# Performance work log

Hardware: AMD Instinct MI355X
Metric: run time of the kernel (lower is better)

Reference implementation:

```python
import jax, jax.numpy as jnp
import numpy as np

B, S, E, D, H = 4, 1024, 1024, 1024, 16   # batch, dec_seq, enc_seq, d_model, n_heads
DH = D // H
DFF = 4096
EPS = 1e-5


def setup_inputs() -> dict:
    key = jax.random.key(0)
    ks = jax.random.split(key, 16)
    w = lambda k, shp: (jax.random.normal(k, shp, dtype=jnp.float32) * 0.02)
    return {
        "x": jax.random.normal(ks[0], (B, S, D), dtype=jnp.float32),
        "enc_x": jax.random.normal(ks[1], (B, E, D), dtype=jnp.float32),
        # masked self-attn (fused qkv)
        "w_qkv": w(ks[2], (D, 3 * D)), "b_qkv": jnp.zeros((3 * D,), jnp.float32),
        "w_sa_o": w(ks[3], (D, D)), "b_sa_o": jnp.zeros((D,), jnp.float32),
        # cross-attn
        "w_q": w(ks[4], (D, D)), "b_q": jnp.zeros((D,), jnp.float32),
        "w_k": w(ks[5], (D, D)), "b_k": jnp.zeros((D,), jnp.float32),
        "w_v": w(ks[6], (D, D)), "b_v": jnp.zeros((D,), jnp.float32),
        "w_ca_o": w(ks[7], (D, D)), "b_ca_o": jnp.zeros((D,), jnp.float32),
        # ffn
        "w1": w(ks[8], (D, DFF)), "b1": jnp.zeros((DFF,), jnp.float32),
        "w2": w(ks[9], (DFF, D)), "b2": jnp.zeros((D,), jnp.float32),
        # layernorms
        "g1": jnp.ones((D,), jnp.float32), "be1": jnp.zeros((D,), jnp.float32),
        "g2": jnp.ones((D,), jnp.float32), "be2": jnp.zeros((D,), jnp.float32),
        "g3": jnp.ones((D,), jnp.float32), "be3": jnp.zeros((D,), jnp.float32),
    }


def _layernorm(x, g, b):
    mean = jnp.mean(x, axis=-1, keepdims=True)
    var = jnp.mean(jnp.square(x - mean), axis=-1, keepdims=True)  # unbiased=False
    return g * (x - mean) / jnp.sqrt(var + EPS) + b


def _masked_self_attn(x, w_qkv, b_qkv, w_o, b_o):
    b, s, d = x.shape
    qkv = x @ w_qkv + b_qkv                            # [b,s,3D]
    # Faithful to torch: view as [b,s,H,3*DH] then chunk last dim (interleaved per-head).
    qkv = qkv.reshape(b, s, H, 3 * DH).transpose(0, 2, 1, 3)   # [b,H,s,3DH]
    q, k, v = jnp.split(qkv, 3, axis=-1)               # each [b,H,s,DH]
    scores = jnp.einsum('bhqd,bhkd->bhqk', q, k) / jnp.sqrt(jnp.float32(DH))
    mask = jnp.triu(jnp.ones((s, s), dtype=bool), k=1)
    scores = jnp.where(mask, -jnp.inf, scores)
    attn = jax.nn.softmax(scores, axis=-1)
    out = jnp.einsum('bhqk,bhkd->bhqd', attn, v)       # [b,H,s,DH]
    out = out.transpose(0, 2, 1, 3).reshape(b, s, d)
    return out @ w_o + b_o


def _cross_attn(dec_x, enc_x, w_q, b_q, w_k, b_k, w_v, b_v, w_o, b_o):
    b, sq, d = dec_x.shape
    sk = enc_x.shape[1]
    q = (dec_x @ w_q + b_q).reshape(b, sq, H, DH).transpose(0, 2, 1, 3)
    k = (enc_x @ w_k + b_k).reshape(b, sk, H, DH).transpose(0, 2, 1, 3)
    v = (enc_x @ w_v + b_v).reshape(b, sk, H, DH).transpose(0, 2, 1, 3)
    scores = jnp.einsum('bhqd,bhkd->bhqk', q, k) / jnp.sqrt(jnp.float32(DH))
    attn = jax.nn.softmax(scores, axis=-1)
    out = jnp.einsum('bhqk,bhkd->bhqd', attn, v).transpose(0, 2, 1, 3).reshape(b, sq, d)
    return out @ w_o + b_o


def reference(x, enc_x, w_qkv, b_qkv, w_sa_o, b_sa_o,
              w_q, b_q, w_k, b_k, w_v, b_v, w_ca_o, b_ca_o,
              w1, b1, w2, b2, g1, be1, g2, be2, g3, be3):
    h = _layernorm(x + _masked_self_attn(x, w_qkv, b_qkv, w_sa_o, b_sa_o), g1, be1)
    h = _layernorm(h + _cross_attn(h, enc_x, w_q, b_q, w_k, b_k, w_v, b_v, w_ca_o, b_ca_o), g2, be2)
    ffn = jax.nn.gelu(h @ w1 + b1, approximate=False) @ w2 + b2  # torch F.gelu default = exact
    return _layernorm(h + ffn, g3, be3)
```

## Files before the change

kernel.cpp:

```cpp
#include <hip/hip_runtime.h>

#define BB 4
#define SS 1024
#define DD 1024
#define HH 16
#define DHH 64
#define DFF 4096
#define MROWS 4096
#define NEG_BIG (-1e30f)
#define LOG2E 1.4426950408889634f
#define SCL_L2E 0.1803368801111244f

typedef float  f32x4  __attribute__((ext_vector_type(4)));
typedef __bf16 bf16x8 __attribute__((ext_vector_type(8)));
typedef __bf16 bf16x4 __attribute__((ext_vector_type(4)));

#define DEV __device__ __forceinline__

DEV void glds16(const __bf16* g, __bf16* l) {
  __builtin_amdgcn_global_load_lds((__attribute__((address_space(1))) void*)(g),
                                   (__attribute__((address_space(3))) void*)(l),
                                   16, 0, 0);
}

DEV float sanit(float v) {
  return fminf(fmaxf(v, -1e30f), 1e30f);
}

DEV float gelu_f(float v) {
  const float z  = fabsf(v) * 0.70710678118654752f;
  const float t  = __builtin_amdgcn_rcpf(1.f + 0.3275911f * z);
  float poly = ((((1.061405429f * t - 1.453152027f) * t + 1.421413741f) * t
                 - 0.284496736f) * t + 0.254829592f) * t;
  float er = 1.f - poly * __expf(-z * z);
  er = copysignf(er, v);
  return 0.5f * v * (1.f + er);
}

__global__ __launch_bounds__(256) void cvt_bf16(const float* __restrict__ src,
                                                __bf16* __restrict__ dst)
{
  const int idx = blockIdx.x * 256 + threadIdx.x;
  const f32x4 v = ((const f32x4*)src)[idx];
  bf16x4 o;
#pragma unroll
  for (int i = 0; i < 4; i++) o[i] = (__bf16)v[i];
  ((bf16x4*)dst)[idx] = o;
}

__global__ __launch_bounds__(256) void wtrans(const float* __restrict__ src,
                                              __bf16* __restrict__ dst,
                                              int K, int N)
{
  __shared__ float t[64][65];
  const int k0 = blockIdx.y * 64, n0 = blockIdx.x * 64;
  const int c = threadIdx.x & 63, r0 = threadIdx.x >> 6;
#pragma unroll
  for (int i = 0; i < 16; i++) {
    const int r = r0 * 16 + i;
    t[r][c] = src[(size_t)(k0 + r) * N + n0 + c];
  }
  __syncthreads();
#pragma unroll
  for (int i = 0; i < 16; i++) {
    const int r = r0 * 16 + i;
    dst[(size_t)(n0 + r) * K + k0 + c] = (__bf16)t[c][r];
  }
}

__global__ __launch_bounds__(256) void vtrans(const __bf16* __restrict__ src,
                                              int stride, int colMul, int colAdd,
                                              __bf16* __restrict__ dst)
{
  __shared__ __bf16 t[64][66];
  const int bh = blockIdx.y, b = bh >> 4, h = bh & 15;
  const int s0 = blockIdx.x * 64;
  const int c = threadIdx.x & 63, r0 = threadIdx.x >> 6;
  const __bf16* sp = src + (size_t)(b * SS) * stride + h * colMul + colAdd;
#pragma unroll
  for (int i = 0; i < 16; i++) {
    const int s = r0 * 16 + i;
    t[s][c] = sp[(size_t)(s0 + s) * stride + c];
  }
  __syncthreads();
  __bf16* dp = dst + (size_t)bh * 64 * 1024;
#pragma unroll
  for (int i = 0; i < 16; i++) {
    const int d = r0 * 16 + i;
    dp[(size_t)d * 1024 + s0 + c] = t[c][d];
  }
}

template<int MODE>
__global__ __launch_bounds__(256) void gemm_bt(
    const __bf16* __restrict__ A, const __bf16* __restrict__ Bt,
    const float* __restrict__ bias, const float* __restrict__ bias2,
    void* __restrict__ Cout, int N, int K)
{
  __shared__ __align__(16) __bf16 As[2][128 * 32];
  __shared__ __align__(16) __bf16 Bs[2][128 * 32];

  const int bm = blockIdx.y * 128, bn = blockIdx.x * 128;
  const int tid = threadIdx.x, wid = tid >> 6, lane = tid & 63;
  const int quad = lane >> 4, ln = lane & 15;

  const __bf16* gA = A  + (size_t)(bm + wid * 32 + (lane >> 2)) * K + (lane & 3) * 8;
  const __bf16* gB = Bt + (size_t)(bn + wid * 32 + (lane >> 2)) * K + (lane & 3) * 8;
  const int soff = (wid * 32) * 32;

  f32x4 acc[4][4];
#pragma unroll
  for (int i = 0; i < 4; i++)
#pragma unroll
    for (int j = 0; j < 4; j++) acc[i][j] = (f32x4){0.f, 0.f, 0.f, 0.f};

  const int wr = (wid >> 1) * 64, wc = (wid & 1) * 64;

#define G_STAGE(buf, kt) do {                                     \
    const int k0_ = (kt) * 32;                                    \
    glds16(gA + k0_,          &As[buf][soff]);                    \
    glds16(gA + 16 * K + k0_, &As[buf][soff + 16 * 32]);          \
    glds16(gB + k0_,          &Bs[buf][soff]);                    \
    glds16(gB + 16 * K + k0_, &Bs[buf][soff + 16 * 32]);          \
  } while (0)

#define G_COMP(buf) do {                                                    \
    bf16x8 af[4], bfr[4];                                                   \
    _Pragma("unroll")                                                       \
    for (int i = 0; i < 4; i++)                                             \
      af[i] = *(const bf16x8*)(&As[buf][(wr + i * 16 + ln) * 32 + quad * 8]); \
    _Pragma("unroll")                                                       \
    for (int j = 0; j < 4; j++)                                             \
      bfr[j] = *(const bf16x8*)(&Bs[buf][(wc + j * 16 + ln) * 32 + quad * 8]); \
    _Pragma("unroll")                                                       \
    for (int i = 0; i < 4; i++)                                             \
      _Pragma("unroll")                                                     \
      for (int j = 0; j < 4; j++)                                           \
        acc[i][j] = __builtin_amdgcn_mfma_f32_16x16x32_bf16(af[i], bfr[j], acc[i][j], 0, 0, 0); \
  } while (0)

  const int nk = K >> 5;
  G_STAGE(0, 0);
  __syncthreads();
  for (int kt = 0; kt < nk; kt += 2) {
    G_STAGE(1, kt + 1);
    G_COMP(0);
    __syncthreads();
    if (kt + 2 < nk) G_STAGE(0, kt + 2);
    G_COMP(1);
    __syncthreads();
  }
#undef G_STAGE
#undef G_COMP

#pragma unroll
  for (int j = 0; j < 4; j++) {
    const int col = bn + wc + j * 16 + ln;
    float bv;
    if (MODE == 4) bv = (col < 1024) ? bias[col] : bias2[col - 1024];
    else           bv = bias[col];
#pragma unroll
    for (int i = 0; i < 4; i++) {
#pragma unroll
      for (int r = 0; r < 4; r++) {
        const int row = bm + wr + i * 16 + quad * 4 + r;
        float v = sanit(acc[i][j][r] + bv);
        if (MODE == 1) v = gelu_f(v);
        if (MODE == 3 && (col % 192) < 64) v *= SCL_L2E;
        if (MODE == 2) ((float*)Cout)[(size_t)row * N + col] = v;
        else           ((__bf16*)Cout)[(size_t)row * N + col] = (__bf16)v;
      }
    }
  }
}

template<int MODE, int SPLIT>
__global__ __launch_bounds__(256) void gemm_bt64(
    const __bf16* __restrict__ A, const __bf16* __restrict__ Bt,
    const float* __restrict__ bias, void* __restrict__ Cout,
    int N, int K)
{
  __shared__ __align__(16) __bf16 As[2][128 * 32];
  __shared__ __align__(16) __bf16 Bs[2][64 * 32];

  const int bm = blockIdx.y * 128, bn = blockIdx.x * 64;
  const int kz = SPLIT ? blockIdx.z : 0;
  const int kOff = SPLIT ? kz * (K >> 1) : 0;
  const int tid = threadIdx.x, wid = tid >> 6, lane = tid & 63;
  const int quad = lane >> 4, ln = lane & 15;

  const __bf16* gA = A  + (size_t)(bm + wid * 32 + (lane >> 2)) * K + (lane & 3) * 8 + kOff;
  const __bf16* gB = Bt + (size_t)(bn + wid * 16 + (lane >> 2)) * K + (lane & 3) * 8 + kOff;
  const int aoff = (wid * 32) * 32;
  const int boff = (wid * 16) * 32;

  f32x4 acc[4][2];
#pragma unroll
  for (int i = 0; i < 4; i++)
#pragma unroll
    for (int j = 0; j < 2; j++) acc[i][j] = (f32x4){0.f, 0.f, 0.f, 0.f};

  const int wr = (wid >> 1) * 64, wc = (wid & 1) * 32;

#define G_STAGE(buf, kt) do {                                     \
    const int k0_ = (kt) * 32;                                    \
    glds16(gA + k0_,          &As[buf][aoff]);                    \
    glds16(gA + 16 * K + k0_, &As[buf][aoff + 16 * 32]);          \
    glds16(gB + k0_,          &Bs[buf][boff]);                    \
  } while (0)

#define G_COMP(buf) do {                                                    \
    bf16x8 af[4], bfr[2];                                                   \
    _Pragma("unroll")                                                       \
    for (int i = 0; i < 4; i++)                                             \
      af[i] = *(const bf16x8*)(&As[buf][(wr + i * 16 + ln) * 32 + quad * 8]); \
    _Pragma("unroll")                                                       \
    for (int j = 0; j < 2; j++)                                             \
      bfr[j] = *(const bf16x8*)(&Bs[buf][(wc + j * 16 + ln) * 32 + quad * 8]); \
    _Pragma("unroll")                                                       \
    for (int i = 0; i < 4; i++)                                             \
      _Pragma("unroll")                                                     \
      for (int j = 0; j < 2; j++)                                           \
        acc[i][j] = __builtin_amdgcn_mfma_f32_16x16x32_bf16(af[i], bfr[j], acc[i][j], 0, 0, 0); \
  } while (0)

  const int nk = (K >> SPLIT) >> 5;
  G_STAGE(0, 0);
  __syncthreads();
  for (int kt = 0; kt < nk; kt += 2) {
    G_STAGE(1, kt + 1);
    G_COMP(0);
    __syncthreads();
    if (kt + 2 < nk) G_STAGE(0, kt + 2);
    G_COMP(1);
    __syncthreads();
  }
#undef G_STAGE
#undef G_COMP

  float* outF = (float*)Cout + (SPLIT ? (size_t)kz * MROWS * N : 0);
#pragma unroll
  for (int j = 0; j < 2; j++) {
    const int col = bn + wc + j * 16 + ln;
    const float bv = (SPLIT && kz) ? 0.f : bias[col];
#pragma unroll
    for (int i = 0; i < 4; i++) {
#pragma unroll
      for (int r = 0; r < 4; r++) {
        const int row = bm + wr + i * 16 + quad * 4 + r;
        float v = sanit(acc[i][j][r] + bv);
        if (MODE == 3) v *= SCL_L2E;
        if (MODE == 2) outF[(size_t)row * N + col] = v;
        else           ((__bf16*)Cout)[(size_t)row * N + col] = (__bf16)v;
      }
    }
  }
}

__global__ __launch_bounds__(256) void attn(
    const __bf16* __restrict__ qp, int qStride, int qMul, int qAdd,
    const __bf16* __restrict__ kp, int kStride, int kMul, int kAdd,
    const __bf16* __restrict__ vt, __bf16* __restrict__ outp, int causal)
{
  __shared__ __align__(16) __bf16 Kt[2][64 * 64];
  __shared__ __align__(16) __bf16 Vt[2][64 * 64];
  __shared__ __align__(16) __bf16 ptl[4][32 * 64];

  const int id = blockIdx.x;
  const int bh = ((id >> 6) << 3) | (id & 7);
  const int qblk = (id >> 3) & 7;
  const int b = bh >> 4, h = bh & 15;
  const int tid = threadIdx.x, wid = tid >> 6, lane = tid & 63;
  const int quad = lane >> 4, ln = lane & 15;
  const int qbase = qblk * 128;
  const int rowb0 = qbase + wid * 32;
  const int rowTop = rowb0 + 31;

  bf16x8 aq[2][2];
#pragma unroll
  for (int rf = 0; rf < 2; ++rf) {
    const __bf16* qr = qp + (size_t)(b * SS + rowb0 + rf * 16 + ln) * qStride
                          + h * qMul + qAdd;
#pragma unroll
    for (int ks = 0; ks < 2; ++ks)
      aq[rf][ks] = *(const bf16x8*)(qr + ks * 32 + quad * 8);
  }

  f32x4 acc[2][4];
#pragma unroll
  for (int rf = 0; rf < 2; ++rf)
#pragma unroll
    for (int nb = 0; nb < 4; ++nb) acc[rf][nb] = (f32x4){0.f, 0.f, 0.f, 0.f};
  float l_r[2][4] = {{0.f,0.f,0.f,0.f},{0.f,0.f,0.f,0.f}};

  const __bf16* kbase = kp + (size_t)(b * SS) * kStride + h * kMul + kAdd;
  const __bf16* vtb = vt + (size_t)bh * 64 * 1024;
  __bf16* ptw = ptl[wid];

  const int kvEnd = causal ? (qbase + 128) : SS;
  const int nT = kvEnd >> 6;

  const int sr = wid * 16 + (lane >> 3);
  const int sq = lane & 7;

#pragma unroll
  for (int p = 0; p < 2; ++p) {
    const int r = sr + p * 8;
    const int qs = (sq ^ (r & 7)) * 8;
    glds16(kbase + (size_t)r * kStride + qs, Kt[0] + (wid * 2 + p) * 512);
    glds16(vtb + (size_t)r * 1024 + qs,      Vt[0] + (wid * 2 + p) * 512);
  }

  for (int t = 0; t < nT; ++t) {
    const int cur = t & 1;
    const int kv0 = t * 64;

    if (t + 1 < nT) {
      const int kn = kv0 + 64;
#pragma unroll
      for (int p = 0; p < 2; ++p) {
        const int r = sr + p * 8;
        const int qs = (sq ^ (r & 7)) * 8;
        glds16(kbase + (size_t)(kn + r) * kStride + qs, Kt[cur ^ 1] + (wid * 2 + p) * 512);
        glds16(vtb + (size_t)r * 1024 + kn + qs,        Vt[cur ^ 1] + (wid * 2 + p) * 512);
      }
      __asm__ volatile("s_waitcnt vmcnt(4)" ::: "memory");
    } else {
      __asm__ volatile("s_waitcnt vmcnt(0)" ::: "memory");
    }
    __builtin_amdgcn_sched_barrier(0);
    __builtin_amdgcn_s_barrier();
    __asm__ volatile("" ::: "memory");
    __builtin_amdgcn_sched_barrier(0);

    if (!causal || kv0 <= rowTop) {
      const __bf16* kt = Kt[cur];
      const __bf16* vv = Vt[cur];

      f32x4 sc[2][4];
      {
        bf16x8 kf[4][2];
#pragma unroll
        for (int c = 0; c < 4; ++c) {
          const int row = c * 16 + ln;
#pragma unroll
          for (int ks = 0; ks < 2; ++ks)
            kf[c][ks] = *(const bf16x8*)(kt + row * 64 + (((ks * 4 + quad) ^ (ln & 7)) * 8));
        }
#pragma unroll
        for (int rf = 0; rf < 2; ++rf)
#pragma unroll
          for (int c = 0; c < 4; ++c) {
            f32x4 s_ = (f32x4){0.f, 0.f, 0.f, 0.f};
            s_ = __builtin_amdgcn_mfma_f32_16x16x32_bf16(aq[rf][0], kf[c][0], s_, 0, 0, 0);
            s_ = __builtin_amdgcn_mfma_f32_16x16x32_bf16(aq[rf][1], kf[c][1], s_, 0, 0, 0);
            sc[rf][c] = s_;
          }
      }

#pragma unroll
      for (int rf = 0; rf < 2; ++rf) {
        const bool doMask = causal && (kv0 + 63 > rowb0 + rf * 16);
#pragma unroll
        for (int r = 0; r < 4; ++r) {
          const int rowg = rowb0 + rf * 16 + quad * 4 + r;
          float p[4];
#pragma unroll
          for (int c = 0; c < 4; ++c) {
            float e = sc[rf][c][r];
            if (doMask && (kv0 + c * 16 + ln > rowg)) e = NEG_BIG;
            p[c] = exp2f(e);
          }
          l_r[rf][r] += (p[0] + p[1]) + (p[2] + p[3]);
          const int m = rf * 16 + quad * 4 + r;
          __bf16* pr = ptw + m * 64;
#pragma unroll
          for (int c = 0; c < 4; ++c) {
            const int col = c * 16 + ln;
            pr[(((col >> 3) ^ (m & 7)) << 3) + (col & 7)] = (__bf16)p[c];
          }
        }
      }
      __asm__ volatile("s_waitcnt lgkmcnt(0)" ::: "memory");
      __builtin_amdgcn_sched_barrier(0);

      {
        bf16x8 pa[2][2];
#pragma unroll
        for (int rf = 0; rf < 2; ++rf) {
          const int m = rf * 16 + ln;
#pragma unroll
          for (int ks = 0; ks < 2; ++ks)
            pa[rf][ks] = *(const bf16x8*)(ptw + m * 64 + (((ks * 4 + quad) ^ (m & 7)) * 8));
        }
#pragma unroll
        for (int nb = 0; nb < 4; ++nb) {
          const int vrow = nb * 16 + ln;
          const bf16x8 vf0 = *(const bf16x8*)(vv + vrow * 64 + (((quad)     ^ (ln & 7)) * 8));
          const bf16x8 vf1 = *(const bf16x8*)(vv + vrow * 64 + (((4 + quad) ^ (ln & 7)) * 8));
#pragma unroll
          for (int rf = 0; rf < 2; ++rf) {
            acc[rf][nb] = __builtin_amdgcn_mfma_f32_16x16x32_bf16(pa[rf][0], vf0, acc[rf][nb], 0, 0, 0);
            acc[rf][nb] = __builtin_amdgcn_mfma_f32_16x16x32_bf16(pa[rf][1], vf1, acc[rf][nb], 0, 0, 0);
          }
        }
      }
    }

    __asm__ volatile("" ::: "memory");
    __builtin_amdgcn_sched_barrier(0);
    __builtin_amdgcn_s_barrier();
  }

#pragma unroll
  for (int rf = 0; rf < 2; ++rf) {
#pragma unroll
    for (int r = 0; r < 4; ++r) {
      float l = l_r[rf][r];
#pragma unroll
      for (int off = 1; off < 16; off <<= 1) l += __shfl_xor(l, off, 64);
      const float inv = 1.f / fmaxf(l, 1e-30f);
      const int rowg = rowb0 + rf * 16 + quad * 4 + r;
      __bf16* op = outp + (size_t)(b * SS + rowg) * DD + h * 64;
#pragma unroll
      for (int nb = 0; nb < 4; ++nb)
        op[nb * 16 + ln] = (__bf16)sanit(acc[rf][nb][r] * inv);
    }
  }
}

__global__ __launch_bounds__(256) void ln_k(
    const float* __restrict__ residf, const float* __restrict__ proj,
    const float* __restrict__ proj2,
    const float* __restrict__ g, const float* __restrict__ be,
    float* __restrict__ outf, __bf16* __restrict__ outb)
{
  const int row = blockIdx.x, tid = threadIdx.x;
  const f32x4 pb = ((const f32x4*)(proj   + (size_t)row * 1024))[tid];
  const f32x4 rb = ((const f32x4*)(residf + (size_t)row * 1024))[tid];
  f32x4 x;
#pragma unroll
  for (int i = 0; i < 4; i++) x[i] = pb[i] + rb[i];
  if (proj2) {
    const f32x4 qb_ = ((const f32x4*)(proj2 + (size_t)row * 1024))[tid];
#pragma unroll
    for (int i = 0; i < 4; i++) x[i] += qb_[i];
  }
#pragma unroll
  for (int i = 0; i < 4; i++)
    x[i] = fminf(fmaxf(x[i], -1e15f), 1e15f);
  float s  = x[0] + x[1] + x[2] + x[3];
  float ss = x[0]*x[0] + x[1]*x[1] + x[2]*x[2] + x[3]*x[3];
#pragma unroll
  for (int off = 1; off < 64; off <<= 1) {
    s  += __shfl_xor(s,  off, 64);
    ss += __shfl_xor(ss, off, 64);
  }
  __shared__ float sm[8];
  if ((tid & 63) == 0) { sm[tid >> 6] = s; sm[4 + (tid >> 6)] = ss; }
  __syncthreads();
  s  = sm[0] + sm[1] + sm[2] + sm[3];
  ss = sm[4] + sm[5] + sm[6] + sm[7];
  const float mean = s * (1.f / 1024.f);
  const float var  = fmaxf(ss * (1.f / 1024.f) - mean * mean, 0.f);
  const float rstd = rsqrtf(var + 1e-5f);
  const int c = tid * 4;
  f32x4 o;
#pragma unroll
  for (int i = 0; i < 4; i++)
    o[i] = g[c + i] * ((x[i] - mean) * rstd) + be[c + i];
  if (outf) ((f32x4*)(outf + (size_t)row * 1024))[tid] = o;
  if (outb) {
    bf16x4 ob;
#pragma unroll
    for (int i = 0; i < 4; i++) ob[i] = (__bf16)o[i];
    ((bf16x4*)(outb + (size_t)row * 1024))[tid] = ob;
  }
}

extern "C" void kernel_launch(void* const* d_in, const int* in_sizes, int n_in,
                              void* d_out, int out_size, void* d_ws, size_t ws_size,
                              hipStream_t stream)
{
  const float* x      = (const float*)d_in[0];
  const float* enc    = (const float*)d_in[1];
  const float* w_qkv  = (const float*)d_in[2];
  const float* b_qkv  = (const float*)d_in[3];
  const float* w_sa_o = (const float*)d_in[4];
  const float* b_sa_o = (const float*)d_in[5];
  const float* w_q    = (const float*)d_in[6];
  const float* b_q    = (const float*)d_in[7];
  const float* w_k    = (const float*)d_in[8];
  const float* b_k    = (const float*)d_in[9];
  const float* w_v    = (const float*)d_in[10];
  const float* b_v    = (const float*)d_in[11];
  const float* w_ca_o = (const float*)d_in[12];
  const float* b_ca_o = (const float*)d_in[13];
  const float* w1     = (const float*)d_in[14];
  const float* b1     = (const float*)d_in[15];
  const float* w2     = (const float*)d_in[16];
  const float* b2     = (const float*)d_in[17];
  const float* g1     = (const float*)d_in[18];
  const float* be1    = (const float*)d_in[19];
  const float* g2     = (const float*)d_in[20];
  const float* be2    = (const float*)d_in[21];
  const float* g3     = (const float*)d_in[22];
  const float* be3    = (const float*)d_in[23];

  const size_t MB = 1024 * 1024;
  char* base = (char*)d_ws;
  __bf16* wqkvT = (__bf16*)(base + 0 * MB);
  __bf16* wsaoT = (__bf16*)(base + 6 * MB);
  __bf16* wqT   = (__bf16*)(base + 8 * MB);
  __bf16* wkvT  = (__bf16*)(base + 10 * MB);
  __bf16* wkT   = (__bf16*)(base + 10 * MB);
  __bf16* wvT   = (__bf16*)(base + 12 * MB);
  __bf16* wcaoT = (__bf16*)(base + 14 * MB);
  __bf16* w1T   = (__bf16*)(base + 0 * MB);
  __bf16* w2T   = (__bf16*)(base + 8 * MB);
  __bf16* xb    = (__bf16*)(base + 16 * MB);
  __bf16* encb  = (__bf16*)(base + 24 * MB);
  __bf16* qkv   = (__bf16*)(base + 32 * MB);
  __bf16* kvb   = (__bf16*)(base + 32 * MB);
  __bf16* qcab  = (__bf16*)(base + 48 * MB);
  __bf16* vt    = (__bf16*)(base + 56 * MB);
  __bf16* mid   = (__bf16*)(base + 32 * MB);
  __bf16* attnb = (__bf16*)(base + 64 * MB);
  float*  proj  = (float*) (base + 72 * MB);
  float*  h1f   = (float*) (base + 88 * MB);
  __bf16* h1b   = (__bf16*)(base + 104 * MB);
  float*  h2f   = (float*) (base + 112 * MB);
  __bf16* h2b   = (__bf16*)(base + 128 * MB);
  __bf16* qb = qkv;
  __bf16* kb = qkv + (size_t)MROWS * 1024;
  __bf16* vb = qkv + (size_t)MROWS * 2048;
  (void)kb; (void)vb; (void)wkT; (void)wvT;

  cvt_bf16<<<4096, 256, 0, stream>>>(x,   xb);
  cvt_bf16<<<4096, 256, 0, stream>>>(enc, encb);
  wtrans<<<dim3(48, 16), 256, 0, stream>>>(w_qkv,  wqkvT, 1024, 3072);
  wtrans<<<dim3(16, 16), 256, 0, stream>>>(w_sa_o, wsaoT, 1024, 1024);
  wtrans<<<dim3(16, 16), 256, 0, stream>>>(w_q,    wqT,   1024, 1024);
  wtrans<<<dim3(16, 16), 256, 0, stream>>>(w_k,    wkT,   1024, 1024);
  wtrans<<<dim3(16, 16), 256, 0, stream>>>(w_v,    wvT,   1024, 1024);
  wtrans<<<dim3(16, 16), 256, 0, stream>>>(w_ca_o, wcaoT, 1024, 1024);

  gemm_bt<3><<<dim3(24, 32), 256, 0, stream>>>(xb, wqkvT, b_qkv, nullptr, qkv, 3072, 1024);
  vtrans<<<dim3(16, 64), 256, 0, stream>>>(qkv, 3072, 192, 128, vt);
  attn<<<512, 256, 0, stream>>>(qkv, 3072, 192, 0,
                                qkv, 3072, 192, 64, vt, attnb, 1);
  gemm_bt64<2,0><<<dim3(16, 32), 256, 0, stream>>>(attnb, wsaoT, b_sa_o, proj, 1024, 1024);
  ln_k<<<4096, 256, 0, stream>>>(x, proj, nullptr, g1, be1, h1f, h1b);

  gemm_bt64<3,0><<<dim3(16, 32), 256, 0, stream>>>(h1b, wqT, b_q, qcab, 1024, 1024);
  gemm_bt<4><<<dim3(16, 32), 256, 0, stream>>>(encb, wkvT, b_k, b_v, kvb, 2048, 1024);
  vtrans<<<dim3(16, 64), 256, 0, stream>>>(kvb, 2048, 64, 1024, vt);
  attn<<<512, 256, 0, stream>>>(qcab, 1024, 64, 0,
                                kvb, 2048, 64, 0, vt, attnb, 0);
  gemm_bt64<2,0><<<dim3(16, 32), 256, 0, stream>>>(attnb, wcaoT, b_ca_o, proj, 1024, 1024);
  ln_k<<<4096, 256, 0, stream>>>(h1f, proj, nullptr, g2, be2, h2f, h2b);

  wtrans<<<dim3(64, 16), 256, 0, stream>>>(w1, w1T, 1024, 4096);
  wtrans<<<dim3(16, 64), 256, 0, stream>>>(w2, w2T, 4096, 1024);
  gemm_bt<1><<<dim3(32, 32), 256, 0, stream>>>(h2b, w1T, b1, nullptr, mid, 4096, 1024);
  gemm_bt64<2,1><<<dim3(16, 32, 2), 256, 0, stream>>>(mid, w2T, b2, proj, 1024, 4096);
  ln_k<<<4096, 256, 0, stream>>>(h2f, proj, proj + (size_t)MROWS * 1024,
                                 g3, be3, (float*)d_out, nullptr);

  (void)in_sizes; (void)n_in; (void)out_size; (void)ws_size;
}
```

Measured before the change: 572.0 us.

## Add 256x256 tiled GEMM with 8 waves for QKV and FFN projections

Adds a 512-thread GEMM kernel that computes 256x256 output tiles with a 64-deep K step. It double-buffers LDS filled by direct global-to-LDS loads, uses an XOR-swizzled LDS layout, interleaves loads with MFMA via explicit waitcnt and barriers, raises wave priority during MFMA, and remaps workgroup IDs across the grid. The kernel replaces the 128-tile GEMMs for the fused QKV projection, FFN up-projection with GELU, and the split-K FFN down-projection, aiming for more data reuse per tile and better latency hiding. In exchange it uses larger LDS and register footprints and launches fewer workgroups: 192 for QKV, 256 for FFN1 and 128 for FFN2. That may leave compute units idle or cause a wave-quantization tail.

```diff
diff --git a/kernel.cpp b/kernel.cpp
--- a/kernel.cpp
+++ b/kernel.cpp
@@ -88,6 +88,150 @@
   for (int i = 0; i < 16; i++) {
     const int d = r0 * 16 + i;
     dp[(size_t)d * 1024 + s0 + c] = t[c][d];
+  }
+}
+
+template<int MODE, int SPLIT>
+__global__ __launch_bounds__(512) void gemm256(
+    const __bf16* __restrict__ A, const __bf16* __restrict__ Bt,
+    const float* __restrict__ bias, void* __restrict__ Cout,
+    int N, int K)
+{
+  __shared__ __align__(16) __bf16 As[2][2][2][128 * 32];
+  __shared__ __align__(16) __bf16 Bs[2][2][2][128 * 32];
+
+  const int gx = gridDim.x;
+  const int nwg = gx * gridDim.y;
+  int idl = blockIdx.x + gx * blockIdx.y;
+  idl = (idl & 7) * (nwg >> 3) + (idl >> 3);
+  const int bn = (idl % gx) * 256, bm = (idl / gx) * 256;
+  const int kz = SPLIT ? blockIdx.z : 0;
+  const int Keff = SPLIT ? (K >> 1) : K;
+  const int kOff = SPLIT ? kz * Keff : 0;
+
+  const int tid = threadIdx.x, wid = tid >> 6, lane = tid & 63;
+  const int quad = lane >> 4, ln = lane & 15;
+  const int wr = (wid >> 2) * 128, wc = (wid & 3) * 64;
+  const int mh = wid >> 2;
+  const int nh = (wid & 3) >> 1;
+  const int rbB = wc & 64;
+  const int sw = ln >> 2;
+
+  const int srow = tid >> 2;
+  const int scol = ((tid & 3) ^ ((tid >> 4) & 3)) * 8;
+  const __bf16* gA = A  + (size_t)(bm + srow) * K + kOff + scol;
+  const __bf16* gB = Bt + (size_t)(bn + srow) * K + kOff + scol;
+  const int dOff = tid * 8;
+
+#define STG(bf_, MATG, MATS, kh_, kt_) do {                                         \
+    glds16(MATG + (size_t)(kt_) * 64 + (kh_) * 32,                 &MATS[bf_][0][kh_][0] + dOff); \
+    glds16(MATG + (size_t)128 * K + (size_t)(kt_) * 64 + (kh_) * 32, &MATS[bf_][1][kh_][0] + dOff); \
+  } while (0)
+
+#define LD_A(dst, p_, i_, ks_) \
+  dst = *(const bf16x8*)(&As[p_][mh][ks_][0] + ((i_) * 16 + ln) * 32 + ((quad ^ sw) * 8))
+#define LD_B(dst, p_, j_, ks_) \
+  dst = *(const bf16x8*)(&Bs[p_][nh][ks_][0] + (rbB + (j_) * 16 + ln) * 32 + ((quad ^ sw) * 8))
+
+  f32x4 acc[8][4];
+#pragma unroll
+  for (int i = 0; i < 8; i++)
+#pragma unroll
+    for (int j = 0; j < 4; j++) acc[i][j] = (f32x4){0.f, 0.f, 0.f, 0.f};
+
+  const int nkt = Keff >> 6;
+  STG(0, gA, As, 0, 0); STG(0, gB, Bs, 0, 0);
+  STG(0, gA, As, 1, 0); STG(0, gB, Bs, 1, 0);
+
+  for (int tt = 0; tt < nkt; ++tt) {
+    const int p = tt & 1, pn = p ^ 1;
+    const int ktn = (tt + 1 < nkt) ? (tt + 1) : tt;
+    bf16x8 af[4], bfr[4];
+
+    STG(pn, gA, As, 0, ktn);
+    asm volatile("s_waitcnt vmcnt(6)" ::: "memory");
+    __builtin_amdgcn_sched_barrier(0);
+    __builtin_amdgcn_s_barrier();
+#pragma unroll
+    for (int j = 0; j < 4; j++) LD_B(bfr[j], p, j, 0);
+#pragma unroll
+    for (int i = 0; i < 4; i++) LD_A(af[i], p, i, 0);
+    asm volatile("s_waitcnt lgkmcnt(0)" ::: "memory");
+    __builtin_amdgcn_sched_barrier(0);
+    __builtin_amdgcn_s_setprio(1);
+#pragma unroll
+    for (int i = 0; i < 4; i++)
+#pragma unroll
+      for (int j = 0; j < 4; j++)
+        acc[i][j] = __builtin_amdgcn_mfma_f32_16x16x32_bf16(af[i], bfr[j], acc[i][j], 0, 0, 0);
+    __builtin_amdgcn_s_setprio(0);
+
+    STG(pn, gB, Bs, 0, ktn);
+#pragma unroll
+    for (int i = 0; i < 4; i++) LD_A(af[i], p, i + 4, 0);
+    asm volatile("s_waitcnt lgkmcnt(0)" ::: "memory");
+    __builtin_amdgcn_sched_barrier(0);
+    __builtin_amdgcn_s_setprio(1);
+#pragma unroll
+    for (int i = 0; i < 4; i++)
+#pragma unroll
+      for (int j = 0; j < 4; j++)
+        acc[i + 4][j] = __builtin_amdgcn_mfma_f32_16x16x32_bf16(af[i], bfr[j], acc[i + 4][j], 0, 0, 0);
+    __builtin_amdgcn_s_setprio(0);
+
+    STG(pn, gA, As, 1, ktn);
+    asm volatile("s_waitcnt vmcnt(6)" ::: "memory");
+    __builtin_amdgcn_sched_barrier(0);
+    __builtin_amdgcn_s_barrier();
+#pragma unroll
+    for (int j = 0; j < 4; j++) LD_B(bfr[j], p, j, 1);
+#pragma unroll
+    for (int i = 0; i < 4; i++) LD_A(af[i], p, i, 1);
+    asm volatile("s_waitcnt lgkmcnt(0)" ::: "memory");
+    __builtin_amdgcn_sched_barrier(0);
+    __builtin_amdgcn_s_setprio(1);
+#pragma unroll
+    for (int i = 0; i < 4; i++)
+#pragma unroll
+      for (int j = 0; j < 4; j++)
+        acc[i][j] = __builtin_amdgcn_mfma_f32_16x16x32_bf16(af[i], bfr[j], acc[i][j], 0, 0, 0);
+    __builtin_amdgcn_s_setprio(0);
+
+    STG(pn, gB, Bs, 1, ktn);
+#pragma unroll
+    for (int i = 0; i < 4; i++) LD_A(af[i], p, i + 4, 1);
+    asm volatile("s_waitcnt lgkmcnt(0)" ::: "memory");
+    __builtin_amdgcn_sched_barrier(0);
+    __builtin_amdgcn_s_setprio(1);
+#pragma unroll
+    for (int i = 0; i < 4; i++)
+#pragma unroll
+      for (int j = 0; j < 4; j++)
+        acc[i + 4][j] = __builtin_amdgcn_mfma_f32_16x16x32_bf16(af[i], bfr[j], acc[i + 4][j], 0, 0, 0);
+    __builtin_amdgcn_s_setprio(0);
+    __builtin_amdgcn_s_barrier();
+  }
+#undef STG
+#undef LD_A
+#undef LD_B
+
+  float* outF = (float*)Cout + (SPLIT ? (size_t)kz * MROWS * N : 0);
+#pragma unroll
+  for (int j = 0; j < 4; j++) {
+    const int col = bn + wc + j * 16 + ln;
+    const float bv = (SPLIT && kz) ? 0.f : bias[col];
+#pragma unroll
+    for (int i = 0; i < 8; i++) {
+#pragma unroll
+      for (int r = 0; r < 4; r++) {
+        const int row = bm + wr + i * 16 + quad * 4 + r;
+        float v = sanit(acc[i][j][r] + bv);
+        if (MODE == 1) v = gelu_f(v);
+        if (MODE == 3 && (col % 192) < 64) v *= SCL_L2E;
+        if (MODE == 2) outF[(size_t)row * N + col] = v;
+        else           ((__bf16*)Cout)[(size_t)row * N + col] = (__bf16)v;
+      }
+    }
   }
 }
 
@@ -174,7 +318,7 @@
   }
 }
 
-template<int MODE, int SPLIT>
+template<int MODE>
 __global__ __launch_bounds__(256) void gemm_bt64(
     const __bf16* __restrict__ A, const __bf16* __restrict__ Bt,
     const float* __restrict__ bias, void* __restrict__ Cout,
@@ -184,13 +328,11 @@
   __shared__ __align__(16) __bf16 Bs[2][64 * 32];
 
   const int bm = blockIdx.y * 128, bn = blockIdx.x * 64;
-  const int kz = SPLIT ? blockIdx.z : 0;
-  const int kOff = SPLIT ? kz * (K >> 1) : 0;
   const int tid = threadIdx.x, wid = tid >> 6, lane = tid & 63;
   const int quad = lane >> 4, ln = lane & 15;
 
-  const __bf16* gA = A  + (size_t)(bm + wid * 32 + (lane >> 2)) * K + (lane & 3) * 8 + kOff;
-  const __bf16* gB = Bt + (size_t)(bn + wid * 16 + (lane >> 2)) * K + (lane & 3) * 8 + kOff;
+  const __bf16* gA = A  + (size_t)(bm + wid * 32 + (lane >> 2)) * K + (lane & 3) * 8;
+  const __bf16* gB = Bt + (size_t)(bn + wid * 16 + (lane >> 2)) * K + (lane & 3) * 8;
   const int aoff = (wid * 32) * 32;
   const int boff = (wid * 16) * 32;
 
@@ -224,7 +366,7 @@
         acc[i][j] = __builtin_amdgcn_mfma_f32_16x16x32_bf16(af[i], bfr[j], acc[i][j], 0, 0, 0); \
   } while (0)
 
-  const int nk = (K >> SPLIT) >> 5;
+  const int nk = K >> 5;
   G_STAGE(0, 0);
   __syncthreads();
   for (int kt = 0; kt < nk; kt += 2) {
@@ -238,11 +380,10 @@
 #undef G_STAGE
 #undef G_COMP
 
-  float* outF = (float*)Cout + (SPLIT ? (size_t)kz * MROWS * N : 0);
 #pragma unroll
   for (int j = 0; j < 2; j++) {
     const int col = bn + wc + j * 16 + ln;
-    const float bv = (SPLIT && kz) ? 0.f : bias[col];
+    const float bv = bias[col];
 #pragma unroll
     for (int i = 0; i < 4; i++) {
 #pragma unroll
@@ -250,7 +391,7 @@
         const int row = bm + wr + i * 16 + quad * 4 + r;
         float v = sanit(acc[i][j][r] + bv);
         if (MODE == 3) v *= SCL_L2E;
-        if (MODE == 2) outF[(size_t)row * N + col] = v;
+        if (MODE == 2) ((float*)Cout)[(size_t)row * N + col] = v;
         else           ((__bf16*)Cout)[(size_t)row * N + col] = (__bf16)v;
       }
     }
@@ -531,10 +672,7 @@
   __bf16* h1b   = (__bf16*)(base + 104 * MB);
   float*  h2f   = (float*) (base + 112 * MB);
   __bf16* h2b   = (__bf16*)(base + 128 * MB);
-  __bf16* qb = qkv;
-  __bf16* kb = qkv + (size_t)MROWS * 1024;
-  __bf16* vb = qkv + (size_t)MROWS * 2048;
-  (void)kb; (void)vb; (void)wkT; (void)wvT;
+  (void)wkT; (void)wvT;
 
   cvt_bf16<<<4096, 256, 0, stream>>>(x,   xb);
   cvt_bf16<<<4096, 256, 0, stream>>>(enc, encb);
@@ -545,25 +683,25 @@
   wtrans<<<dim3(16, 16), 256, 0, stream>>>(w_v,    wvT,   1024, 1024);
   wtrans<<<dim3(16, 16), 256, 0, stream>>>(w_ca_o, wcaoT, 1024, 1024);
 
-  gemm_bt<3><<<dim3(24, 32), 256, 0, stream>>>(xb, wqkvT, b_qkv, nullptr, qkv, 3072, 1024);
+  gemm256<3,0><<<dim3(12, 16), 512, 0, stream>>>(xb, wqkvT, b_qkv, qkv, 3072, 1024);
   vtrans<<<dim3(16, 64), 256, 0, stream>>>(qkv, 3072, 192, 128, vt);
   attn<<<512, 256, 0, stream>>>(qkv, 3072, 192, 0,
                                 qkv, 3072, 192, 64, vt, attnb, 1);
-  gemm_bt64<2,0><<<dim3(16, 32), 256, 0, stream>>>(attnb, wsaoT, b_sa_o, proj, 1024, 1024);
+  gemm_bt64<2><<<dim3(16, 32), 256, 0, stream>>>(attnb, wsaoT, b_sa_o, proj, 1024, 1024);
   ln_k<<<4096, 256, 0, stream>>>(x, proj, nullptr, g1, be1, h1f, h1b);
 
-  gemm_bt64<3,0><<<dim3(16, 32), 256, 0, stream>>>(h1b, wqT, b_q, qcab, 1024, 1024);
+  gemm_bt64<3><<<dim3(16, 32), 256, 0, stream>>>(h1b, wqT, b_q, qcab, 1024, 1024);
   gemm_bt<4><<<dim3(16, 32), 256, 0, stream>>>(encb, wkvT, b_k, b_v, kvb, 2048, 1024);
   vtrans<<<dim3(16, 64), 256, 0, stream>>>(kvb, 2048, 64, 1024, vt);
   attn<<<512, 256, 0, stream>>>(qcab, 1024, 64, 0,
                                 kvb, 2048, 64, 0, vt, attnb, 0);
-  gemm_bt64<2,0><<<dim3(16, 32), 256, 0, stream>>>(attnb, wcaoT, b_ca_o, proj, 1024, 1024);
+  gemm_bt64<2><<<dim3(16, 32), 256, 0, stream>>>(attnb, wcaoT, b_ca_o, proj, 1024, 1024);
   ln_k<<<4096, 256, 0, stream>>>(h1f, proj, nullptr, g2, be2, h2f, h2b);
 
   wtrans<<<dim3(64, 16), 256, 0, stream>>>(w1, w1T, 1024, 4096);
   wtrans<<<dim3(16, 64), 256, 0, stream>>>(w2, w2T, 4096, 1024);
-  gemm_bt<1><<<dim3(32, 32), 256, 0, stream>>>(h2b, w1T, b1, nullptr, mid, 4096, 1024);
-  gemm_bt64<2,1><<<dim3(16, 32, 2), 256, 0, stream>>>(mid, w2T, b2, proj, 1024, 4096);
+  gemm256<1,0><<<dim3(16, 16), 512, 0, stream>>>(h2b, w1T, b1, mid, 4096, 1024);
+  gemm256<2,1><<<dim3(4, 16, 2), 512, 0, stream>>>(mid, w2T, b2, proj, 1024, 4096);
   ln_k<<<4096, 256, 0, stream>>>(h2f, proj, proj + (size_t)MROWS * 1024,
                                  g3, be3, (float*)d_out, nullptr);
 
```

Measured after the change: 576.1 us. About the same (+0.7%).
